# Optimization experiments

Hardware: AMD Instinct MI355X
Metric: run time of the kernel (lower is better)

## Reference

```python
import jax, jax.numpy as jnp
import numpy as np

NUM_HEADS = 4
HEAD_SIZE = 64


def setup_inputs() -> dict:
    key = jax.random.key(0)
    k1, k2, k3, k4 = jax.random.split(key, 4)
    N, M, F = 64, 64, 256
    x = jax.random.normal(k1, (N, N, M, F), dtype=jnp.float32)
    # number of items per set, in [1, M]
    nItem = jax.random.uniform(k2, (N,), dtype=jnp.float32, minval=1.0, maxval=float(M))
    W1 = jax.random.normal(k3, (F, NUM_HEADS * HEAD_SIZE), dtype=jnp.float32) * 0.05
    W2 = jax.random.normal(k4, (NUM_HEADS, 1), dtype=jnp.float32) * 0.05
    return {"x": x, "nItem": nItem, "W1": W1, "W2": W2}


def reference(x, nItem, W1, W2):
    N1, N2, M, F = x.shape
    H, D = NUM_HEADS, HEAD_SIZE
    inv_sqrt_d = 1.0 / jnp.sqrt(jnp.asarray(D, jnp.float32))
    # linear projection -> per-head item features [N,N,H,M,D]
    h = (x @ W1).reshape(N1, N2, M, H, D).transpose(0, 1, 3, 2, 4)
    # h_sw[j, i] == h[i, j]
    h_sw = jnp.swapaxes(h, 0, 1)
    # pairwise item-item scores: relu(x[j,i] @ x[i,j]^T / sqrt(D)) -> [N,N,H,M,M]
    s = jax.nn.relu(jnp.einsum('jihad,jihbd->jihab', h, h_sw) * inv_sqrt_d)
    # sum over both item axes -> [N,N,H]; normalize by nItem[i]*nItem[j]
    scores = s.sum(axis=(3, 4)) / nItem[None, :, None] / nItem[:, None, None]
    # final head mixing -> [N,N,1]
    return scores @ W2
```

## Files before the change

kernel.cpp:

```cpp
#include <hip/hip_runtime.h>
#include <hip/hip_bf16.h>


#define NSET 64
#define MITEM 64
#define FFEAT 256

typedef float f32x4 __attribute__((ext_vector_type(4)));
typedef short bf16x8 __attribute__((ext_vector_type(8)));
typedef unsigned short u16;
typedef u16 u16x4 __attribute__((ext_vector_type(4)));

__device__ __forceinline__ u16 f2bf(float f) {
    __bf16 b = (__bf16)f;
    return __builtin_bit_cast(u16, b);
}
__device__ __forceinline__ f32x4 mfma16(bf16x8 a, bf16x8 b, f32x4 c) {
    return __builtin_amdgcn_mfma_f32_16x16x32_bf16(a, b, c, 0, 0, 0);
}

__global__ void prep_w1t_kernel(const float* __restrict__ w1, u16* __restrict__ w1t) {
    int c = blockIdx.x, k = threadIdx.x;
    w1t[c * 256 + k] = f2bf(w1[k * 256 + c]);
}

__global__ __launch_bounds__(512, 4) void fused_kernel(const float* __restrict__ x,
                                                       const u16* __restrict__ w1t,
                                                       const float* __restrict__ nItem,
                                                       const float* __restrict__ W2,
                                                       float* __restrict__ out) {
    __shared__ u16 BUFA[MITEM][264];
    __shared__ u16 BUFB[MITEM][264];
    __shared__ float red[8];

    int p = 0, rem = blockIdx.x;
    while (rem >= NSET - p) { rem -= NSET - p; ++p; }
    const int q = p + rem;

    const float* xA = x + (size_t)(p * NSET + q) * (MITEM * FFEAT);
    const float* xB = x + (size_t)(q * NSET + p) * (MITEM * FFEAT);

    const int tid  = threadIdx.x;
    const int lane = tid & 63;
    const int wave = tid >> 6;
    const int ar   = lane & 15;
    const int k0   = (lane >> 4) * 8;

    float4 ra[8], rb[8];
#pragma unroll
    for (int u = 0; u < 8; ++u) {
        const int f = u * 2048 + tid * 4;
        ra[u] = *(const float4*)(xA + f);
        rb[u] = *(const float4*)(xB + f);
    }
#pragma unroll
    for (int u = 0; u < 8; ++u) {
        const int f = u * 2048 + tid * 4;
        const int r = f >> 8, c = f & 255;
        u16x4 pa = { f2bf(ra[u].x), f2bf(ra[u].y), f2bf(ra[u].z), f2bf(ra[u].w) };
        u16x4 pb = { f2bf(rb[u].x), f2bf(rb[u].y), f2bf(rb[u].z), f2bf(rb[u].w) };
        *(u16x4*)&BUFA[r][c] = pa;
        *(u16x4*)&BUFB[r][c] = pb;
    }
    __syncthreads();

    const int g   = wave & 3;
    const int sel = wave >> 2;
    u16 (*BUF)[264] = sel ? BUFB : BUFA;

    f32x4 acc[4][4] = {};
#pragma unroll
    for (int kc = 0; kc < 8; ++kc) {
        bf16x8 bu[4], a[4];
#pragma unroll
        for (int u = 0; u < 4; ++u)
            bu[u] = *(const bf16x8*)(w1t + (size_t)(g * 64 + u * 16 + ar) * 256
                                         + kc * 32 + k0);
#pragma unroll
        for (int rt = 0; rt < 4; ++rt)
            a[rt] = *(const bf16x8*)&BUF[rt * 16 + ar][kc * 32 + k0];
#pragma unroll
        for (int u = 0; u < 4; ++u)
#pragma unroll
            for (int rt = 0; rt < 4; ++rt)
                acc[rt][u] = mfma16(a[rt], bu[u], acc[rt][u]);
    }
    __syncthreads();

    const int rj = (lane >> 4) * 4;
#pragma unroll
    for (int rt = 0; rt < 4; ++rt)
#pragma unroll
        for (int u = 0; u < 4; ++u) {
            const int cc = g * 64 + u * 16 + ar;
#pragma unroll
            for (int j = 0; j < 4; ++j)
                BUF[rt * 16 + rj + j][cc] = f2bf(acc[rt][u][j]);
        }
    __syncthreads();

    const int hd = wave & 3, rh = wave >> 2;
    const int hc = hd * 64;
    bf16x8 aS[2][2];
#pragma unroll
    for (int rt = 0; rt < 2; ++rt)
#pragma unroll
        for (int kk = 0; kk < 2; ++kk)
            aS[rt][kk] = *(const bf16x8*)&BUFA[rh * 32 + rt * 16 + ar][hc + kk * 32 + k0];

    float sum = 0.f;
#pragma unroll
    for (int bu = 0; bu < 4; ++bu) {
        bf16x8 b0 = *(const bf16x8*)&BUFB[bu * 16 + ar][hc + k0];
        bf16x8 b1 = *(const bf16x8*)&BUFB[bu * 16 + ar][hc + 32 + k0];
#pragma unroll
        for (int rt = 0; rt < 2; ++rt) {
            f32x4 c = {};
            c = mfma16(aS[rt][0], b0, c);
            c = mfma16(aS[rt][1], b1, c);
            sum += fmaxf(c[0], 0.f) + fmaxf(c[1], 0.f) +
                   fmaxf(c[2], 0.f) + fmaxf(c[3], 0.f);
        }
    }

#pragma unroll
    for (int off = 32; off; off >>= 1) sum += __shfl_xor(sum, off);
    if (lane == 0) red[wave] = sum;
    __syncthreads();
    if (tid == 0) {
        const float nP = nItem[p], nQ = nItem[q];
        float v = 0.f;
#pragma unroll
        for (int h = 0; h < 4; ++h)
            v += ((((red[h] + red[h + 4]) * 0.125f) / nQ) / nP) * W2[h];
        out[p * NSET + q] = v;
        out[q * NSET + p] = v;
    }
}

extern "C" void kernel_launch(void* const* d_in, const int* in_sizes, int n_in,
                              void* d_out, int out_size, void* d_ws, size_t ws_size,
                              hipStream_t stream) {
    const float* x     = (const float*)d_in[0];
    const float* nItem = (const float*)d_in[1];
    const float* W1    = (const float*)d_in[2];
    const float* W2    = (const float*)d_in[3];
    float* out = (float*)d_out;

    u16* w1t = (u16*)d_ws;
    if (ws_size < 131072) return;

    hipLaunchKernelGGL(prep_w1t_kernel, dim3(256), dim3(256), 0, stream, W1, w1t);
    hipLaunchKernelGGL(fused_kernel, dim3(2080), dim3(512), 0, stream,
                       x, w1t, nItem, W2, out);
}
```

Before: 97.95 us.

## Load x rows straight into MFMA A-fragments, skipping the LDS staging pass

Each wave now reads its 16 rows of x directly from global memory into registers, converts them to bf16 and uses them as the MFMA A operand, with the next k-chunk's loads issued one step ahead. This removes the initial LDS store and reload of x plus one barrier. The work split also changes: each wave now computes all 256 output columns for 16 rows instead of 64 columns for 64 rows, so every wave streams the whole w1t matrix. The global x loads are now strided across rows rather than fully contiguous per instruction.

```diff
diff --git a/kernel.cpp b/kernel.cpp
--- a/kernel.cpp
+++ b/kernel.cpp
@@ -9,11 +9,18 @@
 typedef float f32x4 __attribute__((ext_vector_type(4)));
 typedef short bf16x8 __attribute__((ext_vector_type(8)));
 typedef unsigned short u16;
-typedef u16 u16x4 __attribute__((ext_vector_type(4)));
 
 __device__ __forceinline__ u16 f2bf(float f) {
     __bf16 b = (__bf16)f;
     return __builtin_bit_cast(u16, b);
+}
+__device__ __forceinline__ bf16x8 pack8(const float4& a, const float4& b) {
+    bf16x8 r;
+    r[0] = (short)f2bf(a.x); r[1] = (short)f2bf(a.y);
+    r[2] = (short)f2bf(a.z); r[3] = (short)f2bf(a.w);
+    r[4] = (short)f2bf(b.x); r[5] = (short)f2bf(b.y);
+    r[6] = (short)f2bf(b.z); r[7] = (short)f2bf(b.w);
+    return r;
 }
 __device__ __forceinline__ f32x4 mfma16(bf16x8 a, bf16x8 b, f32x4 c) {
     return __builtin_amdgcn_mfma_f32_16x16x32_bf16(a, b, c, 0, 0, 0);
@@ -44,59 +51,42 @@
     const int lane = tid & 63;
     const int wave = tid >> 6;
     const int ar   = lane & 15;
-    const int k0   = (lane >> 4) * 8;
+    const int kg   = lane >> 4;
+    const int k0   = kg * 8;
 
-    float4 ra[8], rb[8];
-#pragma unroll
-    for (int u = 0; u < 8; ++u) {
-        const int f = u * 2048 + tid * 4;
-        ra[u] = *(const float4*)(xA + f);
-        rb[u] = *(const float4*)(xB + f);
-    }
-#pragma unroll
-    for (int u = 0; u < 8; ++u) {
-        const int f = u * 2048 + tid * 4;
-        const int r = f >> 8, c = f & 255;
-        u16x4 pa = { f2bf(ra[u].x), f2bf(ra[u].y), f2bf(ra[u].z), f2bf(ra[u].w) };
-        u16x4 pb = { f2bf(rb[u].x), f2bf(rb[u].y), f2bf(rb[u].z), f2bf(rb[u].w) };
-        *(u16x4*)&BUFA[r][c] = pa;
-        *(u16x4*)&BUFB[r][c] = pb;
-    }
-    __syncthreads();
+    const int rg = wave & 3;
+    const float* xs = (wave < 4) ? xA : xB;
+    u16 (*BUF)[264] = (wave < 4) ? BUFA : BUFB;
+    const float4* xrow = (const float4*)(xs + (size_t)(rg * 16 + ar) * FFEAT);
 
-    const int g   = wave & 3;
-    const int sel = wave >> 2;
-    u16 (*BUF)[264] = sel ? BUFB : BUFA;
-
-    f32x4 acc[4][4] = {};
+    f32x4 acc[16] = {};
+    float4 v0 = xrow[kg * 2], v1 = xrow[kg * 2 + 1];
 #pragma unroll
     for (int kc = 0; kc < 8; ++kc) {
-        bf16x8 bu[4], a[4];
+        bf16x8 a = pack8(v0, v1);
+        if (kc < 7) {
+            v0 = xrow[(kc + 1) * 8 + kg * 2];
+            v1 = xrow[(kc + 1) * 8 + kg * 2 + 1];
+        }
 #pragma unroll
-        for (int u = 0; u < 4; ++u)
-            bu[u] = *(const bf16x8*)(w1t + (size_t)(g * 64 + u * 16 + ar) * 256
-                                         + kc * 32 + k0);
+        for (int u = 0; u < 16; u += 4) {
+            bf16x8 b0 = *(const bf16x8*)(w1t + (size_t)((u + 0) * 16 + ar) * 256 + kc * 32 + k0);
+            bf16x8 b1 = *(const bf16x8*)(w1t + (size_t)((u + 1) * 16 + ar) * 256 + kc * 32 + k0);
+            bf16x8 b2 = *(const bf16x8*)(w1t + (size_t)((u + 2) * 16 + ar) * 256 + kc * 32 + k0);
+            bf16x8 b3 = *(const bf16x8*)(w1t + (size_t)((u + 3) * 16 + ar) * 256 + kc * 32 + k0);
+            acc[u + 0] = mfma16(a, b0, acc[u + 0]);
+            acc[u + 1] = mfma16(a, b1, acc[u + 1]);
+            acc[u + 2] = mfma16(a, b2, acc[u + 2]);
+            acc[u + 3] = mfma16(a, b3, acc[u + 3]);
+        }
+    }
+
+    const int rj = kg * 4;
 #pragma unroll
-        for (int rt = 0; rt < 4; ++rt)
-            a[rt] = *(const bf16x8*)&BUF[rt * 16 + ar][kc * 32 + k0];
+    for (int u = 0; u < 16; ++u)
 #pragma unroll
-        for (int u = 0; u < 4; ++u)
-#pragma unroll
-            for (int rt = 0; rt < 4; ++rt)
-                acc[rt][u] = mfma16(a[rt], bu[u], acc[rt][u]);
-    }
-    __syncthreads();
-
-    const int rj = (lane >> 4) * 4;
-#pragma unroll
-    for (int rt = 0; rt < 4; ++rt)
-#pragma unroll
-        for (int u = 0; u < 4; ++u) {
-            const int cc = g * 64 + u * 16 + ar;
-#pragma unroll
-            for (int j = 0; j < 4; ++j)
-                BUF[rt * 16 + rj + j][cc] = f2bf(acc[rt][u][j]);
-        }
+        for (int j = 0; j < 4; ++j)
+            BUF[rg * 16 + rj + j][u * 16 + ar] = f2bf(acc[u][j]);
     __syncthreads();
 
     const int hd = wave & 3, rh = wave >> 2;
```

Measured after the change: 303.4 us. 210% more time.

## Make fused kernel persistent with register prefetch of next pair's inputs

Applied to the files above, without the earlier changes.

Launches a fixed grid of 512 blocks that loop over the 2080 set pairs with a stride equal to the grid size. While the current pair is being computed, the x tiles for the next pair are loaded into registers, with the A loads issued before the projection GEMM and the B loads before the score stage. This is meant to hide global memory latency and remove per-block launch and ramp-up overhead. The cost is higher register pressure from holding prefetched data alongside the accumulators, which may lower occupancy, and uneven work across blocks since 2080 is not a multiple of 512.

```diff
diff --git a/kernel.cpp b/kernel.cpp
--- a/kernel.cpp
+++ b/kernel.cpp
@@ -5,6 +5,8 @@
 #define NSET 64
 #define MITEM 64
 #define FFEAT 256
+#define NPAIR 2080
+#define NBLK 512
 
 typedef float f32x4 __attribute__((ext_vector_type(4)));
 typedef short bf16x8 __attribute__((ext_vector_type(8)));
@@ -17,6 +19,11 @@
 }
 __device__ __forceinline__ f32x4 mfma16(bf16x8 a, bf16x8 b, f32x4 c) {
     return __builtin_amdgcn_mfma_f32_16x16x32_bf16(a, b, c, 0, 0, 0);
+}
+__device__ __forceinline__ void decode_pair(int idx, int& p, int& q) {
+    p = 0;
+    while (idx >= NSET - p) { idx -= NSET - p; ++p; }
+    q = p + idx;
 }
 
 __global__ void prep_w1t_kernel(const float* __restrict__ w1, u16* __restrict__ w1t) {
@@ -33,108 +40,132 @@
     __shared__ u16 BUFB[MITEM][264];
     __shared__ float red[8];
 
-    int p = 0, rem = blockIdx.x;
-    while (rem >= NSET - p) { rem -= NSET - p; ++p; }
-    const int q = p + rem;
-
-    const float* xA = x + (size_t)(p * NSET + q) * (MITEM * FFEAT);
-    const float* xB = x + (size_t)(q * NSET + p) * (MITEM * FFEAT);
-
     const int tid  = threadIdx.x;
     const int lane = tid & 63;
     const int wave = tid >> 6;
     const int ar   = lane & 15;
-    const int k0   = (lane >> 4) * 8;
+    const int kg   = lane >> 4;
+    const int k0   = kg * 8;
+
+    int idx = blockIdx.x;
 
     float4 ra[8], rb[8];
+    {
+        int p, q; decode_pair(idx, p, q);
+        const float* xA = x + (size_t)(p * NSET + q) * (MITEM * FFEAT);
+        const float* xB = x + (size_t)(q * NSET + p) * (MITEM * FFEAT);
 #pragma unroll
-    for (int u = 0; u < 8; ++u) {
-        const int f = u * 2048 + tid * 4;
-        ra[u] = *(const float4*)(xA + f);
-        rb[u] = *(const float4*)(xB + f);
-    }
-#pragma unroll
-    for (int u = 0; u < 8; ++u) {
-        const int f = u * 2048 + tid * 4;
-        const int r = f >> 8, c = f & 255;
-        u16x4 pa = { f2bf(ra[u].x), f2bf(ra[u].y), f2bf(ra[u].z), f2bf(ra[u].w) };
-        u16x4 pb = { f2bf(rb[u].x), f2bf(rb[u].y), f2bf(rb[u].z), f2bf(rb[u].w) };
-        *(u16x4*)&BUFA[r][c] = pa;
-        *(u16x4*)&BUFB[r][c] = pb;
-    }
-    __syncthreads();
-
-    const int g   = wave & 3;
-    const int sel = wave >> 2;
-    u16 (*BUF)[264] = sel ? BUFB : BUFA;
-
-    f32x4 acc[4][4] = {};
-#pragma unroll
-    for (int kc = 0; kc < 8; ++kc) {
-        bf16x8 bu[4], a[4];
-#pragma unroll
-        for (int u = 0; u < 4; ++u)
-            bu[u] = *(const bf16x8*)(w1t + (size_t)(g * 64 + u * 16 + ar) * 256
-                                         + kc * 32 + k0);
-#pragma unroll
-        for (int rt = 0; rt < 4; ++rt)
-            a[rt] = *(const bf16x8*)&BUF[rt * 16 + ar][kc * 32 + k0];
-#pragma unroll
-        for (int u = 0; u < 4; ++u)
-#pragma unroll
-            for (int rt = 0; rt < 4; ++rt)
-                acc[rt][u] = mfma16(a[rt], bu[u], acc[rt][u]);
-    }
-    __syncthreads();
-
-    const int rj = (lane >> 4) * 4;
-#pragma unroll
-    for (int rt = 0; rt < 4; ++rt)
-#pragma unroll
-        for (int u = 0; u < 4; ++u) {
-            const int cc = g * 64 + u * 16 + ar;
-#pragma unroll
-            for (int j = 0; j < 4; ++j)
-                BUF[rt * 16 + rj + j][cc] = f2bf(acc[rt][u][j]);
-        }
-    __syncthreads();
-
-    const int hd = wave & 3, rh = wave >> 2;
-    const int hc = hd * 64;
-    bf16x8 aS[2][2];
-#pragma unroll
-    for (int rt = 0; rt < 2; ++rt)
-#pragma unroll
-        for (int kk = 0; kk < 2; ++kk)
-            aS[rt][kk] = *(const bf16x8*)&BUFA[rh * 32 + rt * 16 + ar][hc + kk * 32 + k0];
-
-    float sum = 0.f;
-#pragma unroll
-    for (int bu = 0; bu < 4; ++bu) {
-        bf16x8 b0 = *(const bf16x8*)&BUFB[bu * 16 + ar][hc + k0];
-        bf16x8 b1 = *(const bf16x8*)&BUFB[bu * 16 + ar][hc + 32 + k0];
-#pragma unroll
-        for (int rt = 0; rt < 2; ++rt) {
-            f32x4 c = {};
-            c = mfma16(aS[rt][0], b0, c);
-            c = mfma16(aS[rt][1], b1, c);
-            sum += fmaxf(c[0], 0.f) + fmaxf(c[1], 0.f) +
-                   fmaxf(c[2], 0.f) + fmaxf(c[3], 0.f);
+        for (int u = 0; u < 8; ++u) {
+            ra[u] = *(const float4*)(xA + u * 2048 + tid * 4);
+            rb[u] = *(const float4*)(xB + u * 2048 + tid * 4);
         }
     }
 
+    for (;;) {
+        int p, q; decode_pair(idx, p, q);
+
 #pragma unroll
-    for (int off = 32; off; off >>= 1) sum += __shfl_xor(sum, off);
-    if (lane == 0) red[wave] = sum;
-    __syncthreads();
-    if (tid == 0) {
-        const float nP = nItem[p], nQ = nItem[q];
-        float v = 0.f;
+        for (int u = 0; u < 8; ++u) {
+            const int f = u * 2048 + tid * 4;
+            const int r = f >> 8, c = f & 255;
+            u16x4 pa = { f2bf(ra[u].x), f2bf(ra[u].y), f2bf(ra[u].z), f2bf(ra[u].w) };
+            u16x4 pb = { f2bf(rb[u].x), f2bf(rb[u].y), f2bf(rb[u].z), f2bf(rb[u].w) };
+            *(u16x4*)&BUFA[r][c] = pa;
+            *(u16x4*)&BUFB[r][c] = pb;
+        }
+        __syncthreads();
+
+        const int nidx = idx + NBLK;
+        const bool last = nidx >= NPAIR;
+        int lp, lq; decode_pair(last ? idx : nidx, lp, lq);
+        const float* nxA = x + (size_t)(lp * NSET + lq) * (MITEM * FFEAT);
+        const float* nxB = x + (size_t)(lq * NSET + lp) * (MITEM * FFEAT);
+
 #pragma unroll
-        for (int h = 0; h < 4; ++h)
-            v += ((((red[h] + red[h + 4]) * 0.125f) / nQ) / nP) * W2[h];
-        out[p * NSET + q] = v;
-        out[q * NSET + p] = v;
+        for (int u = 0; u < 8; ++u) ra[u] = *(const float4*)(nxA + u * 2048 + tid * 4);
+        __builtin_amdgcn_sched_barrier(0);
+
+        const int g = wave & 3;
+        u16 (*BUF)[264] = (wave < 4) ? BUFA : BUFB;
+        {
+            f32x4 acc[4][4] = {};
+#pragma unroll
+            for (int kc = 0; kc < 8; ++kc) {
+                bf16x8 a[4];
+#pragma unroll
+                for (int rt = 0; rt < 4; ++rt)
+                    a[rt] = *(const bf16x8*)&BUF[rt * 16 + ar][kc * 32 + k0];
+#pragma unroll
+                for (int u = 0; u < 4; ++u) {
+                    bf16x8 bu = *(const bf16x8*)(w1t
+                        + (size_t)(g * 64 + u * 16 + ar) * 256 + kc * 32 + k0);
+#pragma unroll
+                    for (int rt = 0; rt < 4; ++rt)
+                        acc[rt][u] = mfma16(a[rt], bu, acc[rt][u]);
+                }
+            }
+            __syncthreads();
+
+            const int rj = kg * 4;
+#pragma unroll
+            for (int rt = 0; rt < 4; ++rt)
+#pragma unroll
+                for (int u = 0; u < 4; ++u) {
+                    const int cc = g * 64 + u * 16 + ar;
+#pragma unroll
+                    for (int j = 0; j < 4; ++j)
+                        BUF[rt * 16 + rj + j][cc] = f2bf(acc[rt][u][j]);
+                }
+        }
+        __syncthreads();
+
+#pragma unroll
+        for (int u = 0; u < 8; ++u) rb[u] = *(const float4*)(nxB + u * 2048 + tid * 4);
+        __builtin_amdgcn_sched_barrier(0);
+
+        float sum = 0.f;
+        {
+            const int hd = wave & 3, rh = wave >> 2;
+            const int hc = hd * 64;
+            bf16x8 aS[2][2];
+#pragma unroll
+            for (int rt = 0; rt < 2; ++rt)
+#pragma unroll
+                for (int kk = 0; kk < 2; ++kk)
+                    aS[rt][kk] = *(const bf16x8*)
+                        &BUFA[rh * 32 + rt * 16 + ar][hc + kk * 32 + k0];
+#pragma unroll
+            for (int bu = 0; bu < 4; ++bu) {
+                bf16x8 b0 = *(const bf16x8*)&BUFB[bu * 16 + ar][hc + k0];
+                bf16x8 b1 = *(const bf16x8*)&BUFB[bu * 16 + ar][hc + 32 + k0];
+#pragma unroll
+                for (int rt = 0; rt < 2; ++rt) {
+                    f32x4 c = {};
+                    c = mfma16(aS[rt][0], b0, c);
+                    c = mfma16(aS[rt][1], b1, c);
+                    sum += fmaxf(c[0], 0.f) + fmaxf(c[1], 0.f) +
+                           fmaxf(c[2], 0.f) + fmaxf(c[3], 0.f);
+                }
+            }
+        }
+
+#pragma unroll
+        for (int off = 32; off; off >>= 1) sum += __shfl_xor(sum, off);
+        if (lane == 0) red[wave] = sum;
+        __syncthreads();
+        if (tid == 0) {
+            const float nP = nItem[p], nQ = nItem[q];
+            float v = 0.f;
+#pragma unroll
+            for (int h = 0; h < 4; ++h)
+                v += ((((red[h] + red[h + 4]) * 0.125f) / nQ) / nP) * W2[h];
+            out[p * NSET + q] = v;
+            out[q * NSET + p] = v;
+        }
+
+        if (last) break;
+        idx = nidx;
+        __syncthreads();
     }
 }
 
@@ -151,6 +182,6 @@
     if (ws_size < 131072) return;
 
     hipLaunchKernelGGL(prep_w1t_kernel, dim3(256), dim3(256), 0, stream, W1, w1t);
-    hipLaunchKernelGGL(fused_kernel, dim3(2080), dim3(512), 0, stream,
+    hipLaunchKernelGGL(fused_kernel, dim3(NBLK), dim3(512), 0, stream,
                        x, w1t, nItem, W2, out);
 }
```

Measured after the change: 238.2 us. 2.43x slower.

## Split projection into two row halves and prefetch W1 fragments across k-steps

Applied to the files above, without the earlier changes.

The projection GEMM now processes the 64 item rows in two halves of 32, halving the live accumulator registers (32 floats instead of 64) so the 4-blocks-per-CU launch bound is easier to meet without spills. Within each half, the next k-step's W1 fragments are loaded from global memory while the current MFMAs run, hiding L2 latency. In exchange, W1 is read from global twice per wave and an extra block barrier is added between halves. Writing each half back in place is safe because the second half only reads rows the first half did not overwrite.

```diff
diff --git a/kernel.cpp b/kernel.cpp
--- a/kernel.cpp
+++ b/kernel.cpp
@@ -44,82 +44,97 @@
     const int lane = tid & 63;
     const int wave = tid >> 6;
     const int ar   = lane & 15;
-    const int k0   = (lane >> 4) * 8;
+    const int kg   = lane >> 4;
+    const int k0   = kg * 8;
 
-    float4 ra[8], rb[8];
+    {
+        float4 ra[8], rb[8];
 #pragma unroll
-    for (int u = 0; u < 8; ++u) {
-        const int f = u * 2048 + tid * 4;
-        ra[u] = *(const float4*)(xA + f);
-        rb[u] = *(const float4*)(xB + f);
-    }
+        for (int u = 0; u < 8; ++u) {
+            const int f = u * 2048 + tid * 4;
+            ra[u] = *(const float4*)(xA + f);
+            rb[u] = *(const float4*)(xB + f);
+        }
 #pragma unroll
-    for (int u = 0; u < 8; ++u) {
-        const int f = u * 2048 + tid * 4;
-        const int r = f >> 8, c = f & 255;
-        u16x4 pa = { f2bf(ra[u].x), f2bf(ra[u].y), f2bf(ra[u].z), f2bf(ra[u].w) };
-        u16x4 pb = { f2bf(rb[u].x), f2bf(rb[u].y), f2bf(rb[u].z), f2bf(rb[u].w) };
-        *(u16x4*)&BUFA[r][c] = pa;
-        *(u16x4*)&BUFB[r][c] = pb;
+        for (int u = 0; u < 8; ++u) {
+            const int f = u * 2048 + tid * 4;
+            const int r = f >> 8, c = f & 255;
+            u16x4 pa = { f2bf(ra[u].x), f2bf(ra[u].y), f2bf(ra[u].z), f2bf(ra[u].w) };
+            u16x4 pb = { f2bf(rb[u].x), f2bf(rb[u].y), f2bf(rb[u].z), f2bf(rb[u].w) };
+            *(u16x4*)&BUFA[r][c] = pa;
+            *(u16x4*)&BUFB[r][c] = pb;
+        }
     }
     __syncthreads();
 
     const int g   = wave & 3;
     const int sel = wave >> 2;
     u16 (*BUF)[264] = sel ? BUFB : BUFA;
+    const u16* wb = w1t + (size_t)(g * 64 + ar) * 256 + k0;
 
-    f32x4 acc[4][4] = {};
 #pragma unroll
-    for (int kc = 0; kc < 8; ++kc) {
-        bf16x8 bu[4], a[4];
+    for (int un = 0; un < 2; ++un) {
+        f32x4 acc[2][4] = {};
+        bf16x8 bcur[4];
 #pragma unroll
         for (int u = 0; u < 4; ++u)
-            bu[u] = *(const bf16x8*)(w1t + (size_t)(g * 64 + u * 16 + ar) * 256
-                                         + kc * 32 + k0);
+            bcur[u] = *(const bf16x8*)(wb + (size_t)(u * 16) * 256);
 #pragma unroll
-        for (int rt = 0; rt < 4; ++rt)
-            a[rt] = *(const bf16x8*)&BUF[rt * 16 + ar][kc * 32 + k0];
+        for (int kc = 0; kc < 8; ++kc) {
+            bf16x8 a0 = *(const bf16x8*)&BUF[un * 32 +  0 + ar][kc * 32 + k0];
+            bf16x8 a1 = *(const bf16x8*)&BUF[un * 32 + 16 + ar][kc * 32 + k0];
+            bf16x8 bnxt[4];
+            if (kc < 7) {
 #pragma unroll
-        for (int u = 0; u < 4; ++u)
+                for (int u = 0; u < 4; ++u)
+                    bnxt[u] = *(const bf16x8*)(wb + (size_t)(u * 16) * 256
+                                                  + (kc + 1) * 32);
+            }
 #pragma unroll
-            for (int rt = 0; rt < 4; ++rt)
-                acc[rt][u] = mfma16(a[rt], bu[u], acc[rt][u]);
+            for (int u = 0; u < 4; ++u) {
+                acc[0][u] = mfma16(a0, bcur[u], acc[0][u]);
+                acc[1][u] = mfma16(a1, bcur[u], acc[1][u]);
+            }
+#pragma unroll
+            for (int u = 0; u < 4; ++u) bcur[u] = bnxt[u];
+        }
+        __syncthreads();
+
+#pragma unroll
+        for (int rt = 0; rt < 2; ++rt)
+#pragma unroll
+            for (int u = 0; u < 4; ++u) {
+                const int cc = g * 64 + u * 16 + ar;
+#pragma unroll
+                for (int j = 0; j < 4; ++j)
+                    BUF[un * 32 + rt * 16 + kg * 4 + j][cc] = f2bf(acc[rt][u][j]);
+            }
     }
     __syncthreads();
 
-    const int rj = (lane >> 4) * 4;
+    float sum = 0.f;
+    {
+        const int hd = wave & 3, rh = wave >> 2;
+        const int hc = hd * 64;
+        bf16x8 aS[2][2];
 #pragma unroll
-    for (int rt = 0; rt < 4; ++rt)
+        for (int rt = 0; rt < 2; ++rt)
 #pragma unroll
-        for (int u = 0; u < 4; ++u) {
-            const int cc = g * 64 + u * 16 + ar;
+            for (int kk = 0; kk < 2; ++kk)
+                aS[rt][kk] = *(const bf16x8*)
+                    &BUFA[rh * 32 + rt * 16 + ar][hc + kk * 32 + k0];
 #pragma unroll
-            for (int j = 0; j < 4; ++j)
-                BUF[rt * 16 + rj + j][cc] = f2bf(acc[rt][u][j]);
-        }
-    __syncthreads();
-
-    const int hd = wave & 3, rh = wave >> 2;
-    const int hc = hd * 64;
-    bf16x8 aS[2][2];
+        for (int bu = 0; bu < 4; ++bu) {
+            bf16x8 b0 = *(const bf16x8*)&BUFB[bu * 16 + ar][hc + k0];
+            bf16x8 b1 = *(const bf16x8*)&BUFB[bu * 16 + ar][hc + 32 + k0];
 #pragma unroll
-    for (int rt = 0; rt < 2; ++rt)
-#pragma unroll
-        for (int kk = 0; kk < 2; ++kk)
-            aS[rt][kk] = *(const bf16x8*)&BUFA[rh * 32 + rt * 16 + ar][hc + kk * 32 + k0];
-
-    float sum = 0.f;
-#pragma unroll
-    for (int bu = 0; bu < 4; ++bu) {
-        bf16x8 b0 = *(const bf16x8*)&BUFB[bu * 16 + ar][hc + k0];
-        bf16x8 b1 = *(const bf16x8*)&BUFB[bu * 16 + ar][hc + 32 + k0];
-#pragma unroll
-        for (int rt = 0; rt < 2; ++rt) {
-            f32x4 c = {};
-            c = mfma16(aS[rt][0], b0, c);
-            c = mfma16(aS[rt][1], b1, c);
-            sum += fmaxf(c[0], 0.f) + fmaxf(c[1], 0.f) +
-                   fmaxf(c[2], 0.f) + fmaxf(c[3], 0.f);
+            for (int rt = 0; rt < 2; ++rt) {
+                f32x4 c = {};
+                c = mfma16(aS[rt][0], b0, c);
+                c = mfma16(aS[rt][1], b1, c);
+                sum += fmaxf(c[0], 0.f) + fmaxf(c[1], 0.f) +
+                       fmaxf(c[2], 0.f) + fmaxf(c[3], 0.f);
+            }
         }
     }
 
```

Result: slower. 157.8 us (+61.1%).
